# Kernel tuning notes

Measured on AMD Instinct MI355X. Metric: run time of the kernel, lower is better.

The kernel has to match this reference:

```python
import jax, jax.numpy as jnp
import numpy as np

N = 2_097_152  # total atoms
G = 32_768     # number of graphs (~64 atoms each)
EPS = 1e-4     # sign-detection threshold from the original code


def setup_inputs() -> dict:
    key = jax.random.key(0)
    k1, k2 = jax.random.split(key)
    pos = jax.random.normal(k1, (N, 3), dtype=jnp.float32) * 3.0
    batch = jnp.sort(jax.random.randint(k2, (N,), 0, G))
    return {"pos": pos, "batch": batch, "num_graphs": G}


def reference(pos, batch, num_graphs):
    n = pos.shape[0]
    dtype = pos.dtype

    # per-graph centroid (scatter_mean)
    counts = jax.ops.segment_sum(jnp.ones((n,), dtype), batch, num_segments=num_graphs)
    center = jax.ops.segment_sum(pos, batch, num_segments=num_graphs) / jnp.maximum(counts, 1.0)[:, None]
    pc = pos - center[batch]                      # [N,3] centered positions

    # per-atom inertia contribution: r^2 * I - p p^T, then scatter_add per graph
    r_sq = jnp.sum(pc * pc, axis=-1)              # [N]
    outer = jnp.einsum('ni,nj->nij', pc, pc)      # [N,3,3]
    I_atom = r_sq[:, None, None] * jnp.eye(3, dtype=dtype) - outer
    I_mol = jax.ops.segment_sum(I_atom, batch, num_segments=num_graphs)  # [G,3,3]

    L, Q = jnp.linalg.eigh(I_mol)                 # Q: [G,3,3], columns = principal axes

    # projections of centered positions onto the (pre-flip) eigenbasis.
    # NOTE: in the torch loop, p_proj is computed once before any sign flips, and
    # flipping column 0 does not affect p_proj[:,1], so axes 0 and 1 are independent.
    proj = jnp.einsum('ni,nij->nj', pc, Q[batch])  # [N,3]

    idx = jnp.arange(n)

    def axis_sign(a):
        # parallel "first atom (in original order) with |proj| > EPS" per graph
        qual = jnp.abs(proj[:, a]) > EPS
        key_idx = jnp.where(qual, idx, n)
        first = jax.ops.segment_min(key_idx, batch, num_segments=num_graphs)  # [G]
        found = first < n
        val = proj[jnp.minimum(first, n - 1), a]
        return jnp.where(found & (val < 0), -1.0, 1.0).astype(dtype)

    s0 = axis_sign(0)
    s1 = axis_sign(1)
    q0 = Q[:, :, 0] * s0[:, None]
    q1 = Q[:, :, 1] * s1[:, None]
    q2 = jnp.cross(q0, q1)  # enforce right-handed frame
    return jnp.stack([q0, q1, q2], axis=-1)       # [G,3,3]
```

## Files before the change

kernel.cpp:

```cpp
#include <hip/hip_runtime.h>
#include <math.h>

#define CANON_EPS 1e-4f
#define SUBA 16

__global__ void build_starts_kernel(const int* __restrict__ batch,
                                    int* __restrict__ starts, int n, int G) {
  int i = blockIdx.x * blockDim.x + threadIdx.x;
  if (i >= n) return;
  int b = batch[i];
  int bp = (i == 0) ? -1 : batch[i - 1];
  for (int g = bp + 1; g <= b; ++g) starts[g] = i;
  if (i == n - 1) {
    for (int g = b + 1; g <= G; ++g) starts[g] = n;
  }
}

__device__ __forceinline__ float red16(float v) {
  v += __shfl_xor(v, 1);
  v += __shfl_xor(v, 2);
  v += __shfl_xor(v, 4);
  v += __shfl_xor(v, 8);
  return v;
}

__global__ __launch_bounds__(256) void moments_kernel(
    const float* __restrict__ pos, const int* __restrict__ starts,
    float* __restrict__ wsf, int G) {
  int tid = (int)(blockIdx.x * (unsigned)blockDim.x + threadIdx.x);
  int gid = tid / SUBA;
  int sublane = tid & (SUBA - 1);
  if (gid >= G) return;

  int s = starts[gid];
  int e = starts[gid + 1];
  int cnt = e - s;

  float sx = 0.f, sy = 0.f, sz = 0.f;
  float sxx = 0.f, syy = 0.f, szz = 0.f, sxy = 0.f, sxz = 0.f, syz = 0.f;
  for (int i = s + sublane; i < e; i += SUBA) {
    float x = pos[3 * i + 0];
    float y = pos[3 * i + 1];
    float z = pos[3 * i + 2];
    sx += x; sy += y; sz += z;
    sxx = fmaf(x, x, sxx); syy = fmaf(y, y, syy); szz = fmaf(z, z, szz);
    sxy = fmaf(x, y, sxy); sxz = fmaf(x, z, sxz); syz = fmaf(y, z, syz);
  }
  sx = red16(sx); sy = red16(sy); sz = red16(sz);
  sxx = red16(sxx); syy = red16(syy); szz = red16(szz);
  sxy = red16(sxy); sxz = red16(sxz); syz = red16(syz);

  float fn = (float)(cnt > 0 ? cnt : 1);
  float inv = 1.0f / fn;
  float mx = sx * inv, my = sy * inv, mz = sz * inv;
  float Sxx = fmaf(-fn * mx, mx, sxx);
  float Syy = fmaf(-fn * my, my, syy);
  float Szz = fmaf(-fn * mz, mz, szz);
  float Sxy = fmaf(-fn * mx, my, sxy);
  float Sxz = fmaf(-fn * mx, mz, sxz);
  float Syz = fmaf(-fn * my, mz, syz);

  float v = mx;
  v = (sublane == 1) ? my : v;
  v = (sublane == 2) ? mz : v;
  v = (sublane == 3) ? (Syy + Szz) : v;
  v = (sublane == 4) ? (Sxx + Szz) : v;
  v = (sublane == 5) ? (Sxx + Syy) : v;
  v = (sublane == 6) ? (-Sxy) : v;
  v = (sublane == 7) ? (-Sxz) : v;
  v = (sublane == 8) ? (-Syz) : v;
  if (sublane < 9) wsf[sublane * G + gid] = v;
}

__device__ __forceinline__ void jacobi3_f32(float a00, float a11, float a22,
                                            float a01, float a02, float a12,
                                            float Q[3][3]) {
  float A00 = a00, A11 = a11, A22 = a22;
  float A01 = a01, A02 = a02, A12 = a12;
  float Q00 = 1.f, Q01 = 0.f, Q02 = 0.f;
  float Q10 = 0.f, Q11 = 1.f, Q12 = 0.f;
  float Q20 = 0.f, Q21 = 0.f, Q22 = 1.f;

#define ROT(App, Aqq, Apq, Akp, Akq, Qrp0, Qrq0, Qrp1, Qrq1, Qrp2, Qrq2)     \
  {                                                                          \
    float apq = Apq;                                                         \
    float theta = (Aqq - App) / (2.0f * apq);                                \
    float t = copysignf(1.0f, theta) /                                       \
              (fabsf(theta) + sqrtf(1.0f + theta * theta));                  \
    t = (apq == 0.0f) ? 0.0f : t;                    \
    float c = 1.0f / sqrtf(1.0f + t * t);                                    \
    float s = t * c;                                                         \
    App = App - t * apq;                                                     \
    Aqq = Aqq + t * apq;                                                     \
    Apq = 0.0f;                                                              \
    float akp = Akp, akq = Akq;                                              \
    Akp = c * akp - s * akq;                                                 \
    Akq = s * akp + c * akq;                                                 \
    float r0p = Qrp0, r0q = Qrq0;                                            \
    Qrp0 = c * r0p - s * r0q;                                                \
    Qrq0 = s * r0p + c * r0q;                                                \
    float r1p = Qrp1, r1q = Qrq1;                                            \
    Qrp1 = c * r1p - s * r1q;                                                \
    Qrq1 = s * r1p + c * r1q;                                                \
    float r2p = Qrp2, r2q = Qrq2;                                            \
    Qrp2 = c * r2p - s * r2q;                                                \
    Qrq2 = s * r2p + c * r2q;                                                \
  }

#pragma unroll
  for (int sweep = 0; sweep < 5; ++sweep) {
    ROT(A00, A11, A01, A02, A12, Q00, Q01, Q10, Q11, Q20, Q21);
    ROT(A00, A22, A02, A01, A12, Q00, Q02, Q10, Q12, Q20, Q22);
    ROT(A11, A22, A12, A01, A02, Q01, Q02, Q11, Q12, Q21, Q22);
  }
#undef ROT

  float w0 = A00, w1 = A11, w2 = A22;
#define CSWAP(wa, wb, qa0, qb0, qa1, qb1, qa2, qb2)                          \
  {                                                                          \
    bool sw = (wb) < (wa);                                                   \
    float tw = wa; wa = sw ? wb : wa; wb = sw ? tw : wb;                     \
    float t0 = qa0; qa0 = sw ? qb0 : qa0; qb0 = sw ? t0 : qb0;               \
    float t1 = qa1; qa1 = sw ? qb1 : qa1; qb1 = sw ? t1 : qb1;               \
    float t2 = qa2; qa2 = sw ? qb2 : qa2; qb2 = sw ? t2 : qb2;               \
  }
  CSWAP(w0, w1, Q00, Q01, Q10, Q11, Q20, Q21);
  CSWAP(w1, w2, Q01, Q02, Q11, Q12, Q21, Q22);
  CSWAP(w0, w1, Q00, Q01, Q10, Q11, Q20, Q21);
#undef CSWAP

  Q[0][0] = Q00; Q[0][1] = Q01; Q[0][2] = Q02;
  Q[1][0] = Q10; Q[1][1] = Q11; Q[1][2] = Q12;
  Q[2][0] = Q20; Q[2][1] = Q21; Q[2][2] = Q22;
}

__global__ __launch_bounds__(64) void eigen_kernel(
    const float* __restrict__ pos, const int* __restrict__ starts,
    const float* __restrict__ wsf, float* __restrict__ out, int G) {
  int g = (int)(blockIdx.x * (unsigned)blockDim.x + threadIdx.x);
  if (g >= G) return;

  float cx  = wsf[0 * G + g];
  float cy  = wsf[1 * G + g];
  float cz  = wsf[2 * G + g];
  float ixx = wsf[3 * G + g];
  float iyy = wsf[4 * G + g];
  float izz = wsf[5 * G + g];
  float ixy = wsf[6 * G + g];
  float ixz = wsf[7 * G + g];
  float iyz = wsf[8 * G + g];

  float Q[3][3];
  jacobi3_f32(ixx, iyy, izz, ixy, ixz, iyz, Q);

  float q00 = Q[0][0], q10 = Q[1][0], q20 = Q[2][0];
  float q01 = Q[0][1], q11 = Q[1][1], q21 = Q[2][1];

  int s = starts[g];
  int e = starts[g + 1];

  bool found0 = false, found1 = false;
  float v0 = 0.f, v1 = 0.f;
  for (int i = s; i < e; ++i) {
    float x = pos[3 * i + 0] - cx;
    float y = pos[3 * i + 1] - cy;
    float z = pos[3 * i + 2] - cz;
    float p0 = x * q00 + y * q10 + z * q20;
    float p1 = x * q01 + y * q11 + z * q21;
    if (!found0 && fabsf(p0) > CANON_EPS) { v0 = p0; found0 = true; }
    if (!found1 && fabsf(p1) > CANON_EPS) { v1 = p1; found1 = true; }
    if (found0 && found1) break;
  }
  float s0 = (found0 && v0 < 0.f) ? -1.f : 1.f;
  float s1 = (found1 && v1 < 0.f) ? -1.f : 1.f;

  float q0x = q00 * s0, q0y = q10 * s0, q0z = q20 * s0;
  float q1x = q01 * s1, q1y = q11 * s1, q1z = q21 * s1;
  float q2x = q0y * q1z - q0z * q1y;
  float q2y = q0z * q1x - q0x * q1z;
  float q2z = q0x * q1y - q0y * q1x;
  float* o = out + (size_t)g * 9;
  o[0] = q0x; o[1] = q1x; o[2] = q2x;
  o[3] = q0y; o[4] = q1y; o[5] = q2y;
  o[6] = q0z; o[7] = q1z; o[8] = q2z;
}

extern "C" void kernel_launch(void* const* d_in, const int* in_sizes, int n_in,
                              void* d_out, int out_size, void* d_ws, size_t ws_size,
                              hipStream_t stream) {
  const float* pos = (const float*)d_in[0];
  const int* batch = (const int*)d_in[1];
  float* out = (float*)d_out;

  int n = in_sizes[0] / 3;
  int G = out_size / 9;

  int* starts = (int*)d_ws;
  float* wsf = (float*)((char*)d_ws + ((size_t)(G + 1) * 4 + 255 & ~255ull));

  build_starts_kernel<<<(n + 255) / 256, 256, 0, stream>>>(batch, starts, n, G);

  int gperA = 256 / SUBA;
  moments_kernel<<<(G + gperA - 1) / gperA, 256, 0, stream>>>(pos, starts, wsf, G);

  eigen_kernel<<<(G + 63) / 64, 64, 0, stream>>>(pos, starts, wsf, out, G);
}
```

Measured before the change: 23.68 us.

## Replace starts-building kernel with per-graph binary search inside moments kernel

Removes the separate build_starts kernel that read the whole batch array. The moments kernel now finds each graph's segment bounds itself with a binary search over the sorted batch array, sharing the results across lanes by shuffle, and writes the starts for the eigen kernel to reuse. It also cuts the lanes per graph from 16 to 8 and enlarges the eigen kernel's blocks from 64 to 256 threads. This saves one launch and one full pass over batch, at the cost of about 21 dependent scattered loads per graph-boundary lookup.

```diff
diff --git a/kernel.cpp b/kernel.cpp
--- a/kernel.cpp
+++ b/kernel.cpp
@@ -2,43 +2,35 @@
 #include <math.h>
 
 #define CANON_EPS 1e-4f
-#define SUBA 16
-
-__global__ void build_starts_kernel(const int* __restrict__ batch,
-                                    int* __restrict__ starts, int n, int G) {
-  int i = blockIdx.x * blockDim.x + threadIdx.x;
-  if (i >= n) return;
-  int b = batch[i];
-  int bp = (i == 0) ? -1 : batch[i - 1];
-  for (int g = bp + 1; g <= b; ++g) starts[g] = i;
-  if (i == n - 1) {
-    for (int g = b + 1; g <= G; ++g) starts[g] = n;
-  }
-}
-
-__device__ __forceinline__ float red16(float v) {
-  v += __shfl_xor(v, 1);
-  v += __shfl_xor(v, 2);
-  v += __shfl_xor(v, 4);
-  v += __shfl_xor(v, 8);
-  return v;
-}
 
 __global__ __launch_bounds__(256) void moments_kernel(
-    const float* __restrict__ pos, const int* __restrict__ starts,
-    float* __restrict__ wsf, int G) {
+    const float* __restrict__ pos, const int* __restrict__ batch,
+    int* __restrict__ wsi, float* __restrict__ wsf, int n, int G) {
   int tid = (int)(blockIdx.x * (unsigned)blockDim.x + threadIdx.x);
-  int gid = tid / SUBA;
-  int sublane = tid & (SUBA - 1);
+  int gid = tid >> 3;
+  int sub = tid & 7;
+  int lane = (int)(threadIdx.x & 63u);
   if (gid >= G) return;
 
-  int s = starts[gid];
-  int e = starts[gid + 1];
+  int target = gid + (sub & 1);
+  int lo = 0, hi = n;
+  while (lo < hi) {
+    int mid = (lo + hi) >> 1;
+    bool less = batch[mid] < target;
+    lo = less ? mid + 1 : lo;
+    hi = less ? hi : mid;
+  }
+  int base = lane & ~7;
+  int s = __shfl(lo, base);
+  int e = __shfl(lo, base + 1);
+  if (sub == 0) wsi[gid] = s;
+  if (sub == 1 && gid == G - 1) wsi[G] = lo;
+
   int cnt = e - s;
 
   float sx = 0.f, sy = 0.f, sz = 0.f;
   float sxx = 0.f, syy = 0.f, szz = 0.f, sxy = 0.f, sxz = 0.f, syz = 0.f;
-  for (int i = s + sublane; i < e; i += SUBA) {
+  for (int i = s + sub; i < e; i += 8) {
     float x = pos[3 * i + 0];
     float y = pos[3 * i + 1];
     float z = pos[3 * i + 2];
@@ -46,9 +38,12 @@
     sxx = fmaf(x, x, sxx); syy = fmaf(y, y, syy); szz = fmaf(z, z, szz);
     sxy = fmaf(x, y, sxy); sxz = fmaf(x, z, sxz); syz = fmaf(y, z, syz);
   }
-  sx = red16(sx); sy = red16(sy); sz = red16(sz);
-  sxx = red16(sxx); syy = red16(syy); szz = red16(szz);
-  sxy = red16(sxy); sxz = red16(sxz); syz = red16(syz);
+#define RED8(v)                                                              \
+  v += __shfl_xor(v, 1); v += __shfl_xor(v, 2); v += __shfl_xor(v, 4);
+  RED8(sx) RED8(sy) RED8(sz)
+  RED8(sxx) RED8(syy) RED8(szz)
+  RED8(sxy) RED8(sxz) RED8(syz)
+#undef RED8
 
   float fn = (float)(cnt > 0 ? cnt : 1);
   float inv = 1.0f / fn;
@@ -61,15 +56,15 @@
   float Syz = fmaf(-fn * my, mz, syz);
 
   float v = mx;
-  v = (sublane == 1) ? my : v;
-  v = (sublane == 2) ? mz : v;
-  v = (sublane == 3) ? (Syy + Szz) : v;
-  v = (sublane == 4) ? (Sxx + Szz) : v;
-  v = (sublane == 5) ? (Sxx + Syy) : v;
-  v = (sublane == 6) ? (-Sxy) : v;
-  v = (sublane == 7) ? (-Sxz) : v;
-  v = (sublane == 8) ? (-Syz) : v;
-  if (sublane < 9) wsf[sublane * G + gid] = v;
+  v = (sub == 1) ? my : v;
+  v = (sub == 2) ? mz : v;
+  v = (sub == 3) ? (Syy + Szz) : v;
+  v = (sub == 4) ? (Sxx + Szz) : v;
+  v = (sub == 5) ? (Sxx + Syy) : v;
+  v = (sub == 6) ? (-Sxy) : v;
+  v = (sub == 7) ? (-Sxz) : v;
+  wsf[sub * G + gid] = v;
+  if (sub == 0) wsf[8 * G + gid] = -Syz;
 }
 
 __device__ __forceinline__ void jacobi3_f32(float a00, float a11, float a22,
@@ -134,11 +129,14 @@
   Q[2][0] = Q20; Q[2][1] = Q21; Q[2][2] = Q22;
 }
 
-__global__ __launch_bounds__(64) void eigen_kernel(
-    const float* __restrict__ pos, const int* __restrict__ starts,
+__global__ __launch_bounds__(256) void eigen_kernel(
+    const float* __restrict__ pos, const int* __restrict__ wsi,
     const float* __restrict__ wsf, float* __restrict__ out, int G) {
   int g = (int)(blockIdx.x * (unsigned)blockDim.x + threadIdx.x);
   if (g >= G) return;
+
+  int s = wsi[g];
+  int e = wsi[g + 1];
 
   float cx  = wsf[0 * G + g];
   float cy  = wsf[1 * G + g];
@@ -155,9 +153,6 @@
 
   float q00 = Q[0][0], q10 = Q[1][0], q20 = Q[2][0];
   float q01 = Q[0][1], q11 = Q[1][1], q21 = Q[2][1];
-
-  int s = starts[g];
-  int e = starts[g + 1];
 
   bool found0 = false, found1 = false;
   float v0 = 0.f, v1 = 0.f;
@@ -195,13 +190,11 @@
   int n = in_sizes[0] / 3;
   int G = out_size / 9;
 
-  int* starts = (int*)d_ws;
-  float* wsf = (float*)((char*)d_ws + ((size_t)(G + 1) * 4 + 255 & ~255ull));
-
-  build_starts_kernel<<<(n + 255) / 256, 256, 0, stream>>>(batch, starts, n, G);
-
-  int gperA = 256 / SUBA;
-  moments_kernel<<<(G + gperA - 1) / gperA, 256, 0, stream>>>(pos, starts, wsf, G);
-
-  eigen_kernel<<<(G + 63) / 64, 64, 0, stream>>>(pos, starts, wsf, out, G);
-}
+  int* wsi = (int*)d_ws;
+  float* wsf = (float*)((char*)d_ws + (((size_t)(G + 1) * 4 + 255) & ~255ull));
+
+  int blocksA = (G * 8 + 255) / 256;
+  moments_kernel<<<blocksA, 256, 0, stream>>>(pos, batch, wsi, wsf, n, G);
+
+  eigen_kernel<<<(G + 255) / 256, 256, 0, stream>>>(pos, wsi, wsf, out, G);
+}
```

New measurement: 23.46 us. Within noise of the previous version (-0.9%).
